# Kernel optimization log

Measured on AMD Instinct MI355X. Metric: run time of the kernel, lower is better.

## Reference

```python
import jax, jax.numpy as jnp
import numpy as np

N, D = 1048576, 64

def setup_inputs() -> dict:
    key = jax.random.key(0)
    k1, k2, k3 = jax.random.split(key, 3)
    S2_out = jax.random.normal(k1, (N, D), dtype=jnp.float32)
    A1_out = jax.random.normal(k2, (N, D), dtype=jnp.float32)
    labels = jax.random.randint(k3, (N,), 0, 3, dtype=jnp.int64)
    return {"S2_out": S2_out, "A1_out": A1_out, "labels": labels}

def reference(S2_out, A1_out, labels):
    # row-wise L2 distance between A1_out and S2_out (torch.dist(a, b, 2) per row)
    diff = A1_out - S2_out
    d = jnp.sqrt(jnp.sum(diff * diff, axis=-1))  # [N]
    t = jnp.tanh(d)
    # label == 2 -> relu(1 - tanh(d)); otherwise -> relu(1 + tanh(d))
    sign = jnp.where(labels == 2, -1.0, 1.0).astype(S2_out.dtype)
    err = jax.nn.relu(1.0 + sign * t)
    return jnp.sum(err)
```

## Files before the change

### kernel.cpp

```cpp
#include <hip/hip_runtime.h>
#include <hip/hip_bf16.h>


#define BLOCK 256
#define GRID  2048

typedef float fx4 __attribute__((ext_vector_type(4)));

__device__ __forceinline__ fx4 ntload(const fx4* __restrict__ p) {
    return __builtin_nontemporal_load(p);
}

__device__ __forceinline__ float fast_err(float ss, int lab) {
    float d = sqrtf(ss);
    float e = __expf(2.0f * d);
    float t = 1.0f - 2.0f * __builtin_amdgcn_rcpf(e + 1.0f);
    float sgn = (lab == 2) ? -1.0f : 1.0f;
    return fmaxf(fmaf(sgn, t, 1.0f), 0.0f);
}

__device__ __forceinline__ float row_ss(const fx4* __restrict__ A,
                                        const fx4* __restrict__ S,
                                        int row, int l4) {
    const fx4* pa = A + (row << 4) + l4;
    const fx4* ps = S + (row << 4) + l4;
    fx4 a0 = ntload(pa + 0), a1 = ntload(pa + 4), a2 = ntload(pa + 8), a3 = ntload(pa + 12);
    fx4 s0 = ntload(ps + 0), s1 = ntload(ps + 4), s2 = ntload(ps + 8), s3 = ntload(ps + 12);
    float p0, p1, p2, p3, dx;
    dx = a0.x - s0.x; p0 = dx * dx;
    dx = a0.y - s0.y; p0 = fmaf(dx, dx, p0);
    dx = a0.z - s0.z; p0 = fmaf(dx, dx, p0);
    dx = a0.w - s0.w; p0 = fmaf(dx, dx, p0);
    dx = a1.x - s1.x; p1 = dx * dx;
    dx = a1.y - s1.y; p1 = fmaf(dx, dx, p1);
    dx = a1.z - s1.z; p1 = fmaf(dx, dx, p1);
    dx = a1.w - s1.w; p1 = fmaf(dx, dx, p1);
    dx = a2.x - s2.x; p2 = dx * dx;
    dx = a2.y - s2.y; p2 = fmaf(dx, dx, p2);
    dx = a2.z - s2.z; p2 = fmaf(dx, dx, p2);
    dx = a2.w - s2.w; p2 = fmaf(dx, dx, p2);
    dx = a3.x - s3.x; p3 = dx * dx;
    dx = a3.y - s3.y; p3 = fmaf(dx, dx, p3);
    dx = a3.z - s3.z; p3 = fmaf(dx, dx, p3);
    dx = a3.w - s3.w; p3 = fmaf(dx, dx, p3);
    return (p0 + p1) + (p2 + p3);
}

__global__ __launch_bounds__(BLOCK) void loss_antonymy_kernel(
    const fx4* __restrict__ S2,
    const fx4* __restrict__ A1,
    const int* __restrict__ labels,
    float* __restrict__ out,
    int n_rows)
{
    const int tid      = blockIdx.x * BLOCK + threadIdx.x;
    const int group    = tid >> 2;
    const int l4       = threadIdx.x & 3;
    const int n_groups = (GRID * BLOCK) >> 2;

    float acc = 0.0f;

    for (int row = group; row < n_rows; row += 2 * n_groups) {
        const int rowA = row;
        const int rowB = row + n_groups;
        const bool hasB = (rowB < n_rows);

        int labA = labels[rowA];
        int labB = hasB ? labels[rowB] : 0;

        float ssA = row_ss(A1, S2, rowA, l4);
        float ssB = hasB ? row_ss(A1, S2, rowB, l4) : 0.0f;

        ssA += __shfl_xor(ssA, 1, 4);
        ssB += __shfl_xor(ssB, 1, 4);
        ssA += __shfl_xor(ssA, 2, 4);
        ssB += __shfl_xor(ssB, 2, 4);

        float errA = fast_err(ssA, labA);
        float errB = hasB ? fast_err(ssB, labB) : 0.0f;

        if (l4 == 0) acc += errA + errB;
    }

    for (int off = 32; off > 0; off >>= 1)
        acc += __shfl_down(acc, off, 64);

    __shared__ float wsum[BLOCK / 64];
    const int wave = threadIdx.x >> 6;
    const int lane = threadIdx.x & 63;
    if (lane == 0) wsum[wave] = acc;
    __syncthreads();

    if (wave == 0) {
        float v = (lane < (BLOCK / 64)) ? wsum[lane] : 0.0f;
        for (int off = 2; off > 0; off >>= 1)
            v += __shfl_down(v, off, 64);
        if (lane == 0) atomicAdd(out, v);
    }
}

extern "C" void kernel_launch(void* const* d_in, const int* in_sizes, int n_in,
                              void* d_out, int out_size, void* d_ws, size_t ws_size,
                              hipStream_t stream) {
    const fx4* S2     = (const fx4*)d_in[0];
    const fx4* A1     = (const fx4*)d_in[1];
    const int* labels = (const int*)d_in[2];
    float* out = (float*)d_out;

    const int n_rows = in_sizes[2];

    (void)hipMemsetAsync(out, 0, sizeof(float), stream);

    loss_antonymy_kernel<<<GRID, BLOCK, 0, stream>>>(S2, A1, labels, out, n_rows);
}
```

Before: 483.3 us.

## Use 8 lanes per row and two-pass reduction instead of memset plus atomics

Each row is now split across 8 lanes that each load two float4s per tensor, in place of 4 lanes loading four, so memory accesses are more contiguous across a wavefront. The bounds check on the second row is removed, the launch bounds request 8 blocks per CU, and the hipMemset plus global atomicAdd is replaced by per-block partials in workspace and a single-block finalize kernel. This drops the memset launch and atomic contention but adds a second kernel launch, and it assumes n_rows is a multiple of 2*NGROUPS.

```diff
diff --git a/kernel.cpp b/kernel.cpp
--- a/kernel.cpp
+++ b/kernel.cpp
@@ -4,6 +4,7 @@
 
 #define BLOCK 256
 #define GRID  2048
+#define NGROUPS ((GRID * BLOCK) / 8)
 
 typedef float fx4 __attribute__((ext_vector_type(4)));
 
@@ -19,14 +20,14 @@
     return fmaxf(fmaf(sgn, t, 1.0f), 0.0f);
 }
 
-__device__ __forceinline__ float row_ss(const fx4* __restrict__ A,
-                                        const fx4* __restrict__ S,
-                                        int row, int l4) {
-    const fx4* pa = A + (row << 4) + l4;
-    const fx4* ps = S + (row << 4) + l4;
-    fx4 a0 = ntload(pa + 0), a1 = ntload(pa + 4), a2 = ntload(pa + 8), a3 = ntload(pa + 12);
-    fx4 s0 = ntload(ps + 0), s1 = ntload(ps + 4), s2 = ntload(ps + 8), s3 = ntload(ps + 12);
-    float p0, p1, p2, p3, dx;
+__device__ __forceinline__ float row_ss8(const fx4* __restrict__ A,
+                                         const fx4* __restrict__ S,
+                                         int row, int l8) {
+    const fx4* pa = A + (row << 4) + l8;
+    const fx4* ps = S + (row << 4) + l8;
+    fx4 a0 = ntload(pa), a1 = ntload(pa + 8);
+    fx4 s0 = ntload(ps), s1 = ntload(ps + 8);
+    float p0, p1, dx;
     dx = a0.x - s0.x; p0 = dx * dx;
     dx = a0.y - s0.y; p0 = fmaf(dx, dx, p0);
     dx = a0.z - s0.z; p0 = fmaf(dx, dx, p0);
@@ -35,51 +36,43 @@
     dx = a1.y - s1.y; p1 = fmaf(dx, dx, p1);
     dx = a1.z - s1.z; p1 = fmaf(dx, dx, p1);
     dx = a1.w - s1.w; p1 = fmaf(dx, dx, p1);
-    dx = a2.x - s2.x; p2 = dx * dx;
-    dx = a2.y - s2.y; p2 = fmaf(dx, dx, p2);
-    dx = a2.z - s2.z; p2 = fmaf(dx, dx, p2);
-    dx = a2.w - s2.w; p2 = fmaf(dx, dx, p2);
-    dx = a3.x - s3.x; p3 = dx * dx;
-    dx = a3.y - s3.y; p3 = fmaf(dx, dx, p3);
-    dx = a3.z - s3.z; p3 = fmaf(dx, dx, p3);
-    dx = a3.w - s3.w; p3 = fmaf(dx, dx, p3);
-    return (p0 + p1) + (p2 + p3);
+    return p0 + p1;
 }
 
-__global__ __launch_bounds__(BLOCK) void loss_antonymy_kernel(
+__global__ __launch_bounds__(BLOCK, 8) void loss_antonymy_kernel(
     const fx4* __restrict__ S2,
     const fx4* __restrict__ A1,
     const int* __restrict__ labels,
-    float* __restrict__ out,
+    float* __restrict__ partials,
     int n_rows)
 {
-    const int tid      = blockIdx.x * BLOCK + threadIdx.x;
-    const int group    = tid >> 2;
-    const int l4       = threadIdx.x & 3;
-    const int n_groups = (GRID * BLOCK) >> 2;
+    const int tid   = blockIdx.x * BLOCK + threadIdx.x;
+    const int group = tid >> 3;
+    const int l8    = threadIdx.x & 7;
 
     float acc = 0.0f;
 
-    for (int row = group; row < n_rows; row += 2 * n_groups) {
+    for (int row = group; row < n_rows; row += 2 * NGROUPS) {
         const int rowA = row;
-        const int rowB = row + n_groups;
-        const bool hasB = (rowB < n_rows);
+        const int rowB = row + NGROUPS;
 
         int labA = labels[rowA];
-        int labB = hasB ? labels[rowB] : 0;
+        int labB = labels[rowB];
 
-        float ssA = row_ss(A1, S2, rowA, l4);
-        float ssB = hasB ? row_ss(A1, S2, rowB, l4) : 0.0f;
+        float ssA = row_ss8(A1, S2, rowA, l8);
+        float ssB = row_ss8(A1, S2, rowB, l8);
 
-        ssA += __shfl_xor(ssA, 1, 4);
-        ssB += __shfl_xor(ssB, 1, 4);
-        ssA += __shfl_xor(ssA, 2, 4);
-        ssB += __shfl_xor(ssB, 2, 4);
+        ssA += __shfl_xor(ssA, 1, 8);
+        ssB += __shfl_xor(ssB, 1, 8);
+        ssA += __shfl_xor(ssA, 2, 8);
+        ssB += __shfl_xor(ssB, 2, 8);
+        ssA += __shfl_xor(ssA, 4, 8);
+        ssB += __shfl_xor(ssB, 4, 8);
 
         float errA = fast_err(ssA, labA);
-        float errB = hasB ? fast_err(ssB, labB) : 0.0f;
+        float errB = fast_err(ssB, labB);
 
-        if (l4 == 0) acc += errA + errB;
+        if (l8 == 0) acc += errA + errB;
     }
 
     for (int off = 32; off > 0; off >>= 1)
@@ -95,8 +88,28 @@
         float v = (lane < (BLOCK / 64)) ? wsum[lane] : 0.0f;
         for (int off = 2; off > 0; off >>= 1)
             v += __shfl_down(v, off, 64);
-        if (lane == 0) atomicAdd(out, v);
+        if (lane == 0) partials[blockIdx.x] = v;
     }
+}
+
+__global__ __launch_bounds__(256) void finalize_kernel(
+    const float* __restrict__ partials, float* __restrict__ out)
+{
+    float acc = 0.0f;
+    for (int i = threadIdx.x; i < GRID; i += 256)
+        acc += partials[i];
+
+    for (int off = 32; off > 0; off >>= 1)
+        acc += __shfl_down(acc, off, 64);
+
+    __shared__ float wsum[4];
+    const int wave = threadIdx.x >> 6;
+    const int lane = threadIdx.x & 63;
+    if (lane == 0) wsum[wave] = acc;
+    __syncthreads();
+
+    if (threadIdx.x == 0)
+        out[0] = wsum[0] + wsum[1] + wsum[2] + wsum[3];
 }
 
 extern "C" void kernel_launch(void* const* d_in, const int* in_sizes, int n_in,
@@ -105,11 +118,11 @@
     const fx4* S2     = (const fx4*)d_in[0];
     const fx4* A1     = (const fx4*)d_in[1];
     const int* labels = (const int*)d_in[2];
-    float* out = (float*)d_out;
+    float* partials   = (float*)d_ws;
+    float* out        = (float*)d_out;
 
     const int n_rows = in_sizes[2];
 
-    (void)hipMemsetAsync(out, 0, sizeof(float), stream);
-
-    loss_antonymy_kernel<<<GRID, BLOCK, 0, stream>>>(S2, A1, labels, out, n_rows);
+    loss_antonymy_kernel<<<GRID, BLOCK, 0, stream>>>(S2, A1, labels, partials, n_rows);
+    finalize_kernel<<<1, 256, 0, stream>>>(partials, out);
 }
```

Result: no change. 479.2 us (-0.9%).
